# Kernel tuning notes

Measured on AMD Instinct MI355X. Metric: run time of the kernel, lower is better.

Reference implementation:

```python
import jax, jax.numpy as jnp
import numpy as np

RANK = 4
ALPHA = 32
SCALING = ALPHA / RANK  # 8.0
LORA_STRENGTH = 1.0


def setup_inputs() -> dict:
    key = jax.random.key(0)
    ks = jax.random.split(key, 7)
    d_out, d_in = 4096, 4096  # Mistral q/k/v/o_proj weight shape
    batch, seq = 1, 512
    x = jax.random.normal(ks[0], (batch, seq, d_in), dtype=jnp.float32)
    W = jax.random.normal(ks[1], (d_out, d_in), dtype=jnp.float32) * 0.02  # frozen base weight
    A = jax.random.normal(ks[2], (d_out, RANK), dtype=jnp.float32)
    B = jax.random.normal(ks[3], (RANK, d_in), dtype=jnp.float32)
    zc_w = jax.random.normal(ks[4], (), dtype=jnp.float32)  # Conv2d(1,1,1) weight (scalar)
    zc_b = jax.random.normal(ks[5], (), dtype=jnp.float32)  # Conv2d(1,1,1) bias (scalar)
    bias = jax.random.normal(ks[6], (d_out,), dtype=jnp.float32)
    return {"x": x, "W": W, "A": A, "B": B, "zc_w": zc_w, "zc_b": zc_b, "bias": bias}


def reference(x, W, A, B, zc_w, zc_b, bias):
    # low_rank_update = scaling * (A @ B), then 1x1 zero-conv = elementwise scale + bias
    low = SCALING * jnp.einsum('or,ri->oi', A, B)          # [d_out, d_in]
    low = zc_w * low + zc_b                                 # zero_conv (scalar affine)
    W_prime = LORA_STRENGTH * W + low                       # [d_out, d_in]
    # x @ W_prime.T + bias
    return jnp.einsum('bsi,oi->bso', x, W_prime) + bias
```

## Files before the change

kernel.cpp:

```cpp
#include <hip/hip_runtime.h>
#include <hip/hip_bf16.h>


typedef __attribute__((ext_vector_type(8))) short bf16x8;
typedef __attribute__((ext_vector_type(4))) short bf16x4;
typedef __attribute__((ext_vector_type(4))) unsigned short u16x4;
typedef __attribute__((ext_vector_type(4))) float f32x4;

#define MDIM 512
#define NDIM 4096
#define KDIM 4096
#define BM 128
#define BN 128
#define BK 64
#define NT (KDIM / BK)

static __device__ inline unsigned short f2bf(float f) {
  return __bfloat16_as_ushort(__float2bfloat16(f));
}

static __device__ inline bf16x8 pack8(f32x4 a, f32x4 b) {
  bf16x8 v;
  v[0] = (short)f2bf(a[0]); v[1] = (short)f2bf(a[1]);
  v[2] = (short)f2bf(a[2]); v[3] = (short)f2bf(a[3]);
  v[4] = (short)f2bf(b[0]); v[5] = (short)f2bf(b[1]);
  v[6] = (short)f2bf(b[2]); v[7] = (short)f2bf(b[3]);
  return v;
}

static __device__ inline void gll16(const void* g, void* l) {
  __builtin_amdgcn_global_load_lds(
      (const __attribute__((address_space(1))) void*)g,
      (__attribute__((address_space(3))) void*)l, 16, 0, 0);
}

__global__ __launch_bounds__(256) void tk_kernel(
    const float* __restrict__ x, const float* __restrict__ B,
    float* __restrict__ t, float* __restrict__ xs,
    unsigned short* __restrict__ xbf) {
  const int tid = threadIdx.x;
  const int s = blockIdx.x;
  const float* xr = x + (long)s * KDIM;
  float a0 = 0.f, a1 = 0.f, a2 = 0.f, a3 = 0.f, a4 = 0.f;
  for (int k = tid * 4; k < KDIM; k += 1024) {
    f32x4 xv = *(const f32x4*)&xr[k];
    if (xbf) {
      bf16x4 bv;
      bv[0] = (short)f2bf(xv[0]); bv[1] = (short)f2bf(xv[1]);
      bv[2] = (short)f2bf(xv[2]); bv[3] = (short)f2bf(xv[3]);
      *(bf16x4*)&xbf[(long)s * KDIM + k] = bv;
    }
    f32x4 b0 = *(const f32x4*)&B[0 * KDIM + k];
    f32x4 b1 = *(const f32x4*)&B[1 * KDIM + k];
    f32x4 b2 = *(const f32x4*)&B[2 * KDIM + k];
    f32x4 b3 = *(const f32x4*)&B[3 * KDIM + k];
    a0 += xv[0]*b0[0] + xv[1]*b0[1] + xv[2]*b0[2] + xv[3]*b0[3];
    a1 += xv[0]*b1[0] + xv[1]*b1[1] + xv[2]*b1[2] + xv[3]*b1[3];
    a2 += xv[0]*b2[0] + xv[1]*b2[1] + xv[2]*b2[2] + xv[3]*b2[3];
    a3 += xv[0]*b3[0] + xv[1]*b3[1] + xv[2]*b3[2] + xv[3]*b3[3];
    a4 += xv[0] + xv[1] + xv[2] + xv[3];
  }
  #pragma unroll
  for (int off = 32; off; off >>= 1) {
    a0 += __shfl_down(a0, off, 64);
    a1 += __shfl_down(a1, off, 64);
    a2 += __shfl_down(a2, off, 64);
    a3 += __shfl_down(a3, off, 64);
    a4 += __shfl_down(a4, off, 64);
  }
  __shared__ float red[4][5];
  int w = tid >> 6, l = tid & 63;
  if (l == 0) { red[w][0]=a0; red[w][1]=a1; red[w][2]=a2; red[w][3]=a3; red[w][4]=a4; }
  __syncthreads();
  if (tid == 0) {
    t[0 * MDIM + s] = red[0][0] + red[1][0] + red[2][0] + red[3][0];
    t[1 * MDIM + s] = red[0][1] + red[1][1] + red[2][1] + red[3][1];
    t[2 * MDIM + s] = red[0][2] + red[1][2] + red[2][2] + red[3][2];
    t[3 * MDIM + s] = red[0][3] + red[1][3] + red[2][3] + red[3][3];
    xs[s]           = red[0][4] + red[1][4] + red[2][4] + red[3][4];
  }
}

template<int NSPLIT, bool FUSED>
__global__ __launch_bounds__(256) void gemm_v9(
    const unsigned short* __restrict__ xb, const float* __restrict__ W,
    const float* __restrict__ A, const float* __restrict__ bias,
    const float* __restrict__ zcw, const float* __restrict__ zcb,
    const float* __restrict__ t, const float* __restrict__ xs,
    float* __restrict__ dst) {
  __shared__ __align__(16) unsigned short As[2][BM * BK];
  __shared__ __align__(16) unsigned short Ws[2][BN * BK];

  const int bm = blockIdx.x >> 5;
  const int bn = blockIdx.x & 31;
  const int ks = blockIdx.y;
  const int NTloc = NT / NSPLIT;
  const int kbase = ks * (KDIM / NSPLIT);

  const int tid = threadIdx.x;
  const int lane = tid & 63;
  const int wv = tid >> 6;
  const int wm = wv >> 1;
  const int wn = wv & 1;

  const int srow8 = lane >> 3;
  const int schk = (lane & 7) ^ srow8;
  const unsigned short* xsrc[4];
  #pragma unroll
  for (int i = 0; i < 4; ++i)
    xsrc[i] = xb + (long)(bm * BM + i * 32 + wv * 8 + srow8) * KDIM + kbase + schk * 8;

  auto XSTAGE = [&](int kt, int slot) {
    const int koff = kt * BK;
    #pragma unroll
    for (int i = 0; i < 4; ++i)
      gll16(xsrc[i] + koff, &As[slot][i * 2048 + wv * 512]);
  };

  const int wrow = wv * 32 + (lane >> 4);
  const float* wgp = W + (long)(bn * BN + wrow) * KDIM + kbase + (lane & 15) * 4;
  const int wc = (lane & 15) >> 1;
  const int wh = (lane & 1) * 4;

  f32x4 wr[8];
  auto WISSUE = [&](int kt) {
    #pragma unroll
    for (int i = 0; i < 8; ++i)
      wr[i] = *(const f32x4*)(wgp + (long)i * 4 * KDIM + kt * BK);
  };
  auto WWRITE = [&](int slot) {
    #pragma unroll
    for (int i = 0; i < 8; ++i) {
      const int r = wrow + i * 4;
      u16x4 v;
      v[0] = f2bf(wr[i][0]); v[1] = f2bf(wr[i][1]);
      v[2] = f2bf(wr[i][2]); v[3] = f2bf(wr[i][3]);
      *(u16x4*)&Ws[slot][r * 64 + ((wc ^ (r & 7)) << 3) + wh] = v;
    }
  };

  const int fr = lane & 15;
  const int q = lane >> 4;
  const int frs = fr & 7;

  f32x4 acc[4][4] = {};

  auto COMPUTE = [&](int slot) {
    #pragma unroll
    for (int kseg = 0; kseg < 2; ++kseg) {
      const int c = ((kseg * 4 + q) ^ frs) * 8;
      bf16x8 af[4], wf[4];
      #pragma unroll
      for (int mi = 0; mi < 4; ++mi)
        af[mi] = *(const bf16x8*)&As[slot][(wm * 64 + mi * 16 + fr) * 64 + c];
      #pragma unroll
      for (int ni = 0; ni < 4; ++ni)
        wf[ni] = *(const bf16x8*)&Ws[slot][(wn * 64 + ni * 16 + fr) * 64 + c];
      #pragma unroll
      for (int mi = 0; mi < 4; ++mi)
        #pragma unroll
        for (int ni = 0; ni < 4; ++ni)
          acc[mi][ni] = __builtin_amdgcn_mfma_f32_16x16x32_bf16(
              af[mi], wf[ni], acc[mi][ni], 0, 0, 0);
    }
  };

  XSTAGE(0, 0);
  WISSUE(0);
  WWRITE(0);
  __syncthreads();

  for (int kt = 0; kt < NTloc; ++kt) {
    const int cur = kt & 1;
    const int nxt = cur ^ 1;
    if (kt + 1 < NTloc) {
      XSTAGE(kt + 1, nxt);
      WISSUE(kt + 1);
    }
    COMPUTE(cur);
    if (kt + 1 < NTloc) WWRITE(nxt);
    __syncthreads();
  }

  const int s0 = bm * BM + wm * 64;
  const int o0 = bn * BN + wn * 64;
  if (FUSED) {
    const float zw8 = zcw[0] * 8.0f;
    const float zb = zcb[0];
    #pragma unroll
    for (int mi = 0; mi < 4; ++mi) {
      const int sb = s0 + mi * 16 + q * 4;
      f32x4 t0 = *(const f32x4*)&t[0 * MDIM + sb];
      f32x4 t1 = *(const f32x4*)&t[1 * MDIM + sb];
      f32x4 t2 = *(const f32x4*)&t[2 * MDIM + sb];
      f32x4 t3 = *(const f32x4*)&t[3 * MDIM + sb];
      f32x4 x4 = *(const f32x4*)&xs[sb];
      #pragma unroll
      for (int ni = 0; ni < 4; ++ni) {
        const int o = o0 + ni * 16 + fr;
        f32x4 a4 = *(const f32x4*)&A[o * 4];
        const float bo = bias[o];
        #pragma unroll
        for (int j = 0; j < 4; ++j) {
          float corr = zw8 * (a4[0] * t0[j] + a4[1] * t1[j] + a4[2] * t2[j] + a4[3] * t3[j])
                     + zb * x4[j] + bo;
          dst[(long)(sb + j) * NDIM + o] = acc[mi][ni][j] + corr;
        }
      }
    }
  } else {
    float* p = dst + (size_t)ks * MDIM * NDIM;
    #pragma unroll
    for (int mi = 0; mi < 4; ++mi) {
      const int sb = s0 + mi * 16 + q * 4;
      #pragma unroll
      for (int ni = 0; ni < 4; ++ni) {
        const int o = o0 + ni * 16 + fr;
        #pragma unroll
        for (int j = 0; j < 4; ++j)
          p[(long)(sb + j) * NDIM + o] = acc[mi][ni][j];
      }
    }
  }
}

__global__ __launch_bounds__(256) void reduce_kernel(
    const float* __restrict__ p,
    const float* __restrict__ A, const float* __restrict__ bias,
    const float* __restrict__ zcw, const float* __restrict__ zcb,
    const float* __restrict__ t, const float* __restrict__ xs,
    float* __restrict__ out) {
  const long base = ((long)blockIdx.x * 256 + threadIdx.x) * 4;
  const int s = (int)(base / NDIM);
  const int o = (int)(base % NDIM);
  f32x4 v0 = *(const f32x4*)&p[base];
  f32x4 v1 = *(const f32x4*)&p[(long)MDIM * NDIM + base];
  f32x4 v2 = *(const f32x4*)&p[(long)2 * MDIM * NDIM + base];
  f32x4 v3 = *(const f32x4*)&p[(long)3 * MDIM * NDIM + base];
  const float zw8 = zcw[0] * 8.0f;
  const float zb = zcb[0];
  const float t0 = t[0 * MDIM + s], t1 = t[1 * MDIM + s];
  const float t2 = t[2 * MDIM + s], t3 = t[3 * MDIM + s];
  const float xv = xs[s];
  f32x4 bo = *(const f32x4*)&bias[o];
  f32x4 r;
  #pragma unroll
  for (int j = 0; j < 4; ++j) {
    f32x4 a4 = *(const f32x4*)&A[(o + j) * 4];
    r[j] = (v0[j] + v1[j]) + (v2[j] + v3[j])
         + zw8 * (a4[0] * t0 + a4[1] * t1 + a4[2] * t2 + a4[3] * t3)
         + zb * xv + bo[j];
  }
  *(f32x4*)&out[base] = r;
}

__global__ __launch_bounds__(256) void gemm_fallback(
    const float* __restrict__ x, const float* __restrict__ W,
    const float* __restrict__ A, const float* __restrict__ bias,
    const float* __restrict__ zcw, const float* __restrict__ zcb,
    const float* __restrict__ t, const float* __restrict__ xs,
    float* __restrict__ out) {
  __shared__ __align__(16) unsigned short Asf[2][64 * 64];
  __shared__ __align__(16) unsigned short Wsf[2][64 * 64];
  const int bid = blockIdx.x;
  const int bn = bid & 63, bm = bid >> 6;
  const int tid = threadIdx.x, lane = tid & 63, wid = tid >> 6;
  const int wm = wid >> 1, wn = wid & 1;
  const int srow = tid >> 2, sc0 = (tid & 3) * 16;
  const float* xg = x + (long)(bm * 64 + srow) * KDIM + sc0;
  const float* wg = W + (long)(bn * 64 + srow) * KDIM + sc0;
  const int off0 = (srow * 64 + sc0) ^ ((srow & 7) << 3);
  const int off1 = (srow * 64 + sc0 + 8) ^ ((srow & 7) << 3);
  const int fr = lane & 15, fk = (lane >> 4) * 8;
  f32x4 acc[2][2] = {};
  f32x4 xv0, xv1, xv2, xv3, wv0, wv1, wv2, wv3;
  xv0 = *(const f32x4*)(xg);      xv1 = *(const f32x4*)(xg + 4);
  xv2 = *(const f32x4*)(xg + 8);  xv3 = *(const f32x4*)(xg + 12);
  wv0 = *(const f32x4*)(wg);      wv1 = *(const f32x4*)(wg + 4);
  wv2 = *(const f32x4*)(wg + 8);  wv3 = *(const f32x4*)(wg + 12);
  *(bf16x8*)&Asf[0][off0] = pack8(xv0, xv1);
  *(bf16x8*)&Asf[0][off1] = pack8(xv2, xv3);
  *(bf16x8*)&Wsf[0][off0] = pack8(wv0, wv1);
  *(bf16x8*)&Wsf[0][off1] = pack8(wv2, wv3);
  __syncthreads();
  for (int kt = 0; kt < KDIM / 64; ++kt) {
    const int cur = kt & 1;
    if (kt + 1 < KDIM / 64) {
      const int off = (kt + 1) * 64;
      xv0 = *(const f32x4*)(xg + off);      xv1 = *(const f32x4*)(xg + off + 4);
      xv2 = *(const f32x4*)(xg + off + 8);  xv3 = *(const f32x4*)(xg + off + 12);
      wv0 = *(const f32x4*)(wg + off);      wv1 = *(const f32x4*)(wg + off + 4);
      wv2 = *(const f32x4*)(wg + off + 8);  wv3 = *(const f32x4*)(wg + off + 12);
    }
    #pragma unroll
    for (int kss = 0; kss < 2; ++kss) {
      const int kk = kss * 32 + fk;
      const int ra0 = wm * 32 + fr, ra1 = ra0 + 16;
      const int rb0 = wn * 32 + fr, rb1 = rb0 + 16;
      bf16x8 a0 = *(const bf16x8*)&Asf[cur][(ra0 * 64 + kk) ^ ((ra0 & 7) << 3)];
      bf16x8 a1 = *(const bf16x8*)&Asf[cur][(ra1 * 64 + kk) ^ ((ra1 & 7) << 3)];
      bf16x8 b0 = *(const bf16x8*)&Wsf[cur][(rb0 * 64 + kk) ^ ((rb0 & 7) << 3)];
      bf16x8 b1 = *(const bf16x8*)&Wsf[cur][(rb1 * 64 + kk) ^ ((rb1 & 7) << 3)];
      acc[0][0] = __builtin_amdgcn_mfma_f32_16x16x32_bf16(a0, b0, acc[0][0], 0, 0, 0);
      acc[0][1] = __builtin_amdgcn_mfma_f32_16x16x32_bf16(a0, b1, acc[0][1], 0, 0, 0);
      acc[1][0] = __builtin_amdgcn_mfma_f32_16x16x32_bf16(a1, b0, acc[1][0], 0, 0, 0);
      acc[1][1] = __builtin_amdgcn_mfma_f32_16x16x32_bf16(a1, b1, acc[1][1], 0, 0, 0);
    }
    if (kt + 1 < KDIM / 64) {
      const int nxt = cur ^ 1;
      *(bf16x8*)&Asf[nxt][off0] = pack8(xv0, xv1);
      *(bf16x8*)&Asf[nxt][off1] = pack8(xv2, xv3);
      *(bf16x8*)&Wsf[nxt][off0] = pack8(wv0, wv1);
      *(bf16x8*)&Wsf[nxt][off1] = pack8(wv2, wv3);
    }
    __syncthreads();
  }
  const float zw8 = zcw[0] * 8.0f;
  const float zb = zcb[0];
  const int s0 = bm * 64 + wm * 32;
  const int o0 = bn * 64 + wn * 32;
  #pragma unroll
  for (int mi = 0; mi < 2; ++mi) {
    const int sb = s0 + mi * 16 + ((lane >> 4) * 4);
    f32x4 t0 = *(const f32x4*)&t[0 * MDIM + sb];
    f32x4 t1 = *(const f32x4*)&t[1 * MDIM + sb];
    f32x4 t2 = *(const f32x4*)&t[2 * MDIM + sb];
    f32x4 t3 = *(const f32x4*)&t[3 * MDIM + sb];
    f32x4 x4 = *(const f32x4*)&xs[sb];
    #pragma unroll
    for (int ni = 0; ni < 2; ++ni) {
      const int o = o0 + ni * 16 + fr;
      f32x4 a4 = *(const f32x4*)&A[o * 4];
      const float bo = bias[o];
      #pragma unroll
      for (int j = 0; j < 4; ++j) {
        float corr = zw8 * (a4[0] * t0[j] + a4[1] * t1[j] + a4[2] * t2[j] + a4[3] * t3[j])
                   + zb * x4[j] + bo;
        out[(long)(sb + j) * NDIM + o] = acc[mi][ni][j] + corr;
      }
    }
  }
}

extern "C" void kernel_launch(void* const* d_in, const int* in_sizes, int n_in,
                              void* d_out, int out_size, void* d_ws, size_t ws_size,
                              hipStream_t stream) {
  const float* x    = (const float*)d_in[0];
  const float* W    = (const float*)d_in[1];
  const float* A    = (const float*)d_in[2];
  const float* B    = (const float*)d_in[3];
  const float* zcw  = (const float*)d_in[4];
  const float* zcb  = (const float*)d_in[5];
  const float* bias = (const float*)d_in[6];
  float* out = (float*)d_out;

  float* t  = (float*)d_ws;
  float* xs = t + 4 * MDIM;
  unsigned short* xbf = (unsigned short*)(t + 4096);
  float* pbuf = (float*)(xbf + (size_t)MDIM * KDIM);

  const size_t need_x = 4096u * 4 + (size_t)MDIM * KDIM * 2;
  const size_t need_p = need_x + (size_t)4 * MDIM * NDIM * 4;

  if (ws_size >= need_p) {
    tk_kernel<<<MDIM, 256, 0, stream>>>(x, B, t, xs, xbf);
    gemm_v9<4, false><<<dim3(4 * 32, 4), 256, 0, stream>>>(
        xbf, W, A, bias, zcw, zcb, t, xs, pbuf);
    reduce_kernel<<<(MDIM * NDIM) / (4 * 256), 256, 0, stream>>>(
        pbuf, A, bias, zcw, zcb, t, xs, out);
  } else if (ws_size >= need_x) {
    tk_kernel<<<MDIM, 256, 0, stream>>>(x, B, t, xs, xbf);
    gemm_v9<1, true><<<dim3(4 * 32, 1), 256, 0, stream>>>(
        xbf, W, A, bias, zcw, zcb, t, xs, out);
  } else {
    tk_kernel<<<MDIM, 256, 0, stream>>>(x, B, t, xs, nullptr);
    gemm_fallback<<<(MDIM / 64) * (NDIM / 64), 256, 0, stream>>>(
        x, W, A, bias, zcw, zcb, t, xs, out);
  }
}
```

Measured before the change: 51.82 us.

## Prefetch W two tiles ahead with double register buffers and manual waitcnt

The GEMM main loop now keeps two register buffers for the fp32 W tile, so global loads for tile kt+2 are issued while tile kt+1 is converted to bf16 and tile kt is computed. W loads go through inline asm, and synchronisation uses explicit vmcnt/lgkmcnt waits, raw s_barrier and sched_barrier instead of __syncthreads. The loop is unrolled by two with a hand-written epilogue. The aim is to hide HBM latency for W behind MFMA work. It costs more registers and depends on getting the vmcnt counts exactly right.

```diff
diff --git a/kernel.cpp b/kernel.cpp
--- a/kernel.cpp
+++ b/kernel.cpp
@@ -14,6 +14,10 @@
 #define BN 128
 #define BK 64
 #define NT (KDIM / BK)
+
+#define VMCNT(n) asm volatile("s_waitcnt vmcnt(" #n ")" ::: "memory")
+#define LGKM0()  asm volatile("s_waitcnt lgkmcnt(0)" ::: "memory")
+#define SCHED0() __builtin_amdgcn_sched_barrier(0)
 
 static __device__ inline unsigned short f2bf(float f) {
   return __bfloat16_as_ushort(__float2bfloat16(f));
@@ -82,7 +86,7 @@
 }
 
 template<int NSPLIT, bool FUSED>
-__global__ __launch_bounds__(256) void gemm_v9(
+__global__ __launch_bounds__(256) void gemm_v10(
     const unsigned short* __restrict__ xb, const float* __restrict__ W,
     const float* __restrict__ A, const float* __restrict__ bias,
     const float* __restrict__ zcw, const float* __restrict__ zcb,
@@ -122,13 +126,17 @@
   const int wc = (lane & 15) >> 1;
   const int wh = (lane & 1) * 4;
 
-  f32x4 wr[8];
-  auto WISSUE = [&](int kt) {
-    #pragma unroll
-    for (int i = 0; i < 8; ++i)
-      wr[i] = *(const f32x4*)(wgp + (long)i * 4 * KDIM + kt * BK);
+  f32x4 wrA[8], wrB[8];
+  auto WISSUE = [&](f32x4 (&wr)[8], int kt) {
+    const float* base = wgp + kt * BK;
+    #pragma unroll
+    for (int i = 0; i < 8; ++i) {
+      const float* p = base + (long)i * 4 * KDIM;
+      asm volatile("global_load_dwordx4 %0, %1, off"
+                   : "=v"(wr[i]) : "v"(p) : "memory");
+    }
   };
-  auto WWRITE = [&](int slot) {
+  auto WWRITE = [&](const f32x4 (&wr)[8], int slot) {
     #pragma unroll
     for (int i = 0; i < 8; ++i) {
       const int r = wrow + i * 4;
@@ -165,22 +173,40 @@
     }
   };
 
+  WISSUE(wrA, 0);
   XSTAGE(0, 0);
-  WISSUE(0);
-  WWRITE(0);
-  __syncthreads();
-
-  for (int kt = 0; kt < NTloc; ++kt) {
-    const int cur = kt & 1;
-    const int nxt = cur ^ 1;
-    if (kt + 1 < NTloc) {
-      XSTAGE(kt + 1, nxt);
-      WISSUE(kt + 1);
-    }
-    COMPUTE(cur);
-    if (kt + 1 < NTloc) WWRITE(nxt);
-    __syncthreads();
-  }
+  WISSUE(wrB, 1);
+  VMCNT(12); SCHED0();
+  WWRITE(wrA, 0);
+  VMCNT(8);
+  LGKM0();
+  __builtin_amdgcn_s_barrier();
+  SCHED0();
+
+  auto BODY = [&](int kt, const f32x4 (&bCon)[8], f32x4 (&bFill)[8]) {
+    XSTAGE(kt + 1, (kt + 1) & 1);
+    WISSUE(bFill, kt + 2);
+    VMCNT(12); SCHED0();
+    WWRITE(bCon, (kt + 1) & 1);
+    COMPUTE(kt & 1);
+    VMCNT(8);
+    LGKM0();
+    __builtin_amdgcn_s_barrier();
+    SCHED0();
+  };
+  for (int kt = 0; kt < NTloc - 2; kt += 2) {
+    BODY(kt, wrB, wrA);
+    BODY(kt + 1, wrA, wrB);
+  }
+  XSTAGE(NTloc - 1, (NTloc - 1) & 1);
+  VMCNT(4); SCHED0();
+  WWRITE(wrB, (NTloc - 1) & 1);
+  COMPUTE((NTloc - 2) & 1);
+  VMCNT(0);
+  LGKM0();
+  __builtin_amdgcn_s_barrier();
+  SCHED0();
+  COMPUTE((NTloc - 1) & 1);
 
   const int s0 = bm * BM + wm * 64;
   const int o0 = bn * BN + wn * 64;
@@ -364,13 +390,13 @@
 
   if (ws_size >= need_p) {
     tk_kernel<<<MDIM, 256, 0, stream>>>(x, B, t, xs, xbf);
-    gemm_v9<4, false><<<dim3(4 * 32, 4), 256, 0, stream>>>(
+    gemm_v10<4, false><<<dim3(4 * 32, 4), 256, 0, stream>>>(
         xbf, W, A, bias, zcw, zcb, t, xs, pbuf);
     reduce_kernel<<<(MDIM * NDIM) / (4 * 256), 256, 0, stream>>>(
         pbuf, A, bias, zcw, zcb, t, xs, out);
   } else if (ws_size >= need_x) {
     tk_kernel<<<MDIM, 256, 0, stream>>>(x, B, t, xs, xbf);
-    gemm_v9<1, true><<<dim3(4 * 32, 1), 256, 0, stream>>>(
+    gemm_v10<1, true><<<dim3(4 * 32, 1), 256, 0, stream>>>(
         xbf, W, A, bias, zcw, zcb, t, xs, out);
   } else {
     tk_kernel<<<MDIM, 256, 0, stream>>>(x, B, t, xs, nullptr);
```

Result: faster. 46.09 us (-11.1%).
